# Performance work log

Hardware: AMD Instinct MI355X
Metric: run time of the kernel (lower is better)

The kernel has to match this reference:

```python
import jax, jax.numpy as jnp
from jax import lax
import numpy as np

B, T, D_IN, H, OUT = 64, 512, 512, 1024, 128


def setup_inputs() -> dict:
    key = jax.random.key(0)
    ks = jax.random.split(key, 12)
    s = 0.02
    return {
        "x": jax.random.normal(ks[0], (B, T, D_IN), dtype=jnp.float32),
        "W_ih0": jax.random.normal(ks[1], (H, D_IN), dtype=jnp.float32) * s,
        "W_hh0": jax.random.normal(ks[2], (H, H), dtype=jnp.float32) * s,
        "b_ih0": jax.random.normal(ks[3], (H,), dtype=jnp.float32) * s,
        "b_hh0": jax.random.normal(ks[4], (H,), dtype=jnp.float32) * s,
        "W_ih1": jax.random.normal(ks[5], (H, H), dtype=jnp.float32) * s,
        "W_hh1": jax.random.normal(ks[6], (H, H), dtype=jnp.float32) * s,
        "b_ih1": jax.random.normal(ks[7], (H,), dtype=jnp.float32) * s,
        "b_hh1": jax.random.normal(ks[8], (H,), dtype=jnp.float32) * s,
        "W_fc": jax.random.normal(ks[9], (OUT, H), dtype=jnp.float32) * s,
        "b_fc": jax.random.normal(ks[10], (OUT,), dtype=jnp.float32) * s,
    }


def _rnn_layer(seq, W_ih, W_hh, b_ih, b_hh):
    # seq: [B, T, D] -> outputs [B, T, H]; h_t = tanh(x_t W_ih^T + b_ih + h_{t-1} W_hh^T + b_hh)
    pre = jnp.einsum("btd,hd->bth", seq, W_ih) + b_ih + b_hh  # one big input GEMM
    h0 = jnp.zeros((seq.shape[0], W_hh.shape[0]), dtype=seq.dtype)

    def step(h, p_t):
        h_new = jnp.tanh(p_t + h @ W_hh.T)
        return h_new, h_new

    _, hs = lax.scan(step, h0, jnp.swapaxes(pre, 0, 1))  # [T, B, H]
    return jnp.swapaxes(hs, 0, 1)  # [B, T, H]


def reference(x, W_ih0, W_hh0, b_ih0, b_hh0, W_ih1, W_hh1, b_ih1, b_hh1, W_fc, b_fc):
    h1 = _rnn_layer(x, W_ih0, W_hh0, b_ih0, b_hh0)
    h2 = _rnn_layer(h1, W_ih1, W_hh1, b_ih1, b_hh1)
    last = h2[:, -1, :]  # [B, H]
    return last @ W_fc.T + b_fc  # [B, OUT]
```

## Files before the change

kernel.cpp:

```cpp
#include <hip/hip_runtime.h>
#include <stdint.h>
#include <stddef.h>

#define Bn   64
#define Tn   512
#define DINn 512
#define Hn   1024
#define OUTn 128

typedef __attribute__((ext_vector_type(4))) float f32x4;
typedef __attribute__((ext_vector_type(8))) short short8;
typedef __attribute__((ext_vector_type(4))) unsigned int u32x4;

__device__ __forceinline__ unsigned short f2bf(float f){
  unsigned int x = __builtin_bit_cast(unsigned int, f);
  x += 0x7fffu + ((x >> 16) & 1u);
  return (unsigned short)(x >> 16);
}
__device__ __forceinline__ float bf2f(unsigned short u){
  return __builtin_bit_cast(float, (unsigned int)u << 16);
}
__device__ __forceinline__ float tanh_fast(float v){
  float e = __expf(2.0f * v);
  return 1.0f - 2.0f / (e + 1.0f);
}

template<bool FAST>
__device__ __forceinline__ void st16(unsigned short* p, u32x4 v){
  if constexpr (FAST)
    asm volatile("global_store_dwordx4 %0, %1, off sc0" :: "v"(p), "v"(v) : "memory");
  else
    asm volatile("global_store_dwordx4 %0, %1, off sc0 sc1" :: "v"(p), "v"(v) : "memory");
}
__device__ __forceinline__ unsigned atom_poll(unsigned int* p){
  unsigned old, zero = 0;
  asm volatile("global_atomic_add %0, %1, %2, off sc0\n\t"
               "s_waitcnt vmcnt(0)"
               : "=&v"(old) : "v"(p), "v"(zero) : "memory");
  return old;
}
__device__ __forceinline__ void atom_poll2(unsigned int* p1, unsigned int* p2,
                                           unsigned &v1, unsigned &v2){
  unsigned zero = 0;
  asm volatile("global_atomic_add %0, %2, %4, off sc0\n\t"
               "global_atomic_add %1, %3, %4, off sc0\n\t"
               "s_waitcnt vmcnt(0)"
               : "=&v"(v1), "=&v"(v2)
               : "v"(p1), "v"(p2), "v"(zero) : "memory");
}
__device__ __forceinline__ void atom_inc(unsigned int* p){
  unsigned one = 1;
  asm volatile("global_atomic_add %0, %1, off" :: "v"(p), "v"(one) : "memory");
}
__device__ __forceinline__ unsigned ld1_sc0(const unsigned int* p){
  unsigned v;
  asm volatile("global_load_dword %0, %1, off sc0\n\t"
               "s_waitcnt vmcnt(0)" : "=&v"(v) : "v"(p) : "memory");
  return v;
}
__device__ __forceinline__ unsigned ld1_nt(const unsigned int* p){
  unsigned v;
  asm volatile("global_load_dword %0, %1, off nt\n\t"
               "s_waitcnt vmcnt(0)" : "=&v"(v) : "v"(p) : "memory");
  return v;
}
__device__ __forceinline__ void ld2_nt(const unsigned int* p1, const unsigned int* p2,
                                       unsigned &v1, unsigned &v2){
  asm volatile("global_load_dword %0, %2, off nt\n\t"
               "global_load_dword %1, %3, off nt\n\t"
               "s_waitcnt vmcnt(0)"
               : "=&v"(v1), "=&v"(v2) : "v"(p1), "v"(p2) : "memory");
}
__device__ __forceinline__ unsigned umin4(u32x4 a){
  unsigned m0 = a[0] < a[1] ? a[0] : a[1];
  unsigned m1 = a[2] < a[3] ? a[2] : a[3];
  return m0 < m1 ? m0 : m1;
}
__device__ __forceinline__ unsigned ld_line8_slow(const unsigned int* p){
  u32x4 a, b;
  asm volatile("global_load_dwordx4 %0, %2, off sc0 sc1\n\t"
               "global_load_dwordx4 %1, %3, off sc0 sc1\n\t"
               "s_waitcnt vmcnt(0)"
               : "=&v"(a), "=&v"(b) : "v"(p), "v"(p + 4) : "memory");
  unsigned ma = umin4(a), mb = umin4(b);
  return ma < mb ? ma : mb;
}
__device__ __forceinline__ void waitw_nt(const unsigned int* p, unsigned want){
  if (!want) return;
  for (int i = 0; i < (1 << 16); ++i){
    if (ld1_nt(p) >= want) return;
    if (i > 16) __builtin_amdgcn_s_sleep(1);
  }
}
__device__ __forceinline__ void waitw_nt2(const unsigned int* p1, unsigned w1,
                                          const unsigned int* p2, unsigned w2){
  if (!w1){ waitw_nt(p2, w2); return; }
  for (int i = 0; i < (1 << 16); ++i){
    unsigned v1, v2;
    ld2_nt(p1, p2, v1, v2);
    if (v1 >= w1 && v2 >= w2) return;
    if (i > 16) __builtin_amdgcn_s_sleep(1);
  }
}
template<bool FAST>
__device__ __forceinline__ void wait_one(unsigned int* fc, unsigned int* fl, unsigned wfast, unsigned wslow){
  if constexpr (FAST){
    if (!wfast) return;
    for (int i = 0; i < (1 << 16); ++i){
      if (atom_poll(fc) >= wfast) return;
      if (i > 8) __builtin_amdgcn_s_sleep(1);
    }
  } else {
    if (!wslow) return;
    for (int i = 0; i < (1 << 16); ++i){
      if (ld_line8_slow(fl) >= wslow) return;
      if (i > 16) __builtin_amdgcn_s_sleep(1);
    }
  }
}
template<bool FAST>
__device__ __forceinline__ void wait_dual(unsigned int* fc1, unsigned int* fl1, unsigned wf1, unsigned ws1,
                                          unsigned int* fc2, unsigned int* fl2, unsigned wf2, unsigned ws2){
  if constexpr (FAST){
    if (!wf2){ wait_one<true>(fc1, fl1, wf1, ws1); return; }
    for (int i = 0; i < (1 << 16); ++i){
      unsigned v1, v2;
      atom_poll2(fc1, fc2, v1, v2);
      if (v1 >= wf1 && v2 >= wf2) return;
      if (i > 8) __builtin_amdgcn_s_sleep(1);
    }
  } else {
    if (!ws2){ wait_one<false>(fc1, fl1, wf1, ws1); return; }
    for (int i = 0; i < (1 << 16); ++i){
      if (ld_line8_slow(fl1) >= ws1 && ld_line8_slow(fl2) >= ws2) return;
      if (i > 16) __builtin_amdgcn_s_sleep(1);
    }
  }
}

__device__ __forceinline__ void stage_pw(const unsigned short* src, unsigned short* dst, int lane){
  const unsigned short* p0 = src + lane*8;
  const unsigned short* p1 = p0 + 512;
  u32x4 v0, v1;
  asm volatile("global_load_dwordx4 %0, %2, off sc0\n\t"
               "global_load_dwordx4 %1, %3, off sc0\n\t"
               "s_waitcnt vmcnt(0)"
               : "=&v"(v0), "=&v"(v1) : "v"(p0), "v"(p1) : "memory");
  *(u32x4*)(dst + lane*8) = v0;
  *(u32x4*)(dst + lane*8 + 512) = v1;
}
__device__ __forceinline__ void stage_pw_pv(const unsigned short* src, unsigned short* dst, int lane,
                                            const unsigned short* p4, float* pv){
  const unsigned short* p0 = src + lane*8;
  const unsigned short* p1 = p0 + 512;
  u32x4 v0, v1; unsigned u0,u1,u2,u3;
  asm volatile(
    "global_load_dwordx4 %0, %6, off sc0\n\t"
    "global_load_dwordx4 %1, %7, off sc0\n\t"
    "global_load_ushort %2, %8, off sc0\n\t"
    "global_load_ushort %3, %9, off sc0\n\t"
    "global_load_ushort %4, %10, off sc0\n\t"
    "global_load_ushort %5, %11, off sc0\n\t"
    "s_waitcnt vmcnt(0)"
    : "=&v"(v0),"=&v"(v1),"=&v"(u0),"=&v"(u1),"=&v"(u2),"=&v"(u3)
    : "v"(p0),"v"(p1),"v"(p4),"v"(p4+8),"v"(p4+16),"v"(p4+24) : "memory");
  *(u32x4*)(dst + lane*8) = v0;
  *(u32x4*)(dst + lane*8 + 512) = v1;
  pv[0]=bf2f((unsigned short)u0); pv[1]=bf2f((unsigned short)u1);
  pv[2]=bf2f((unsigned short)u2); pv[3]=bf2f((unsigned short)u3);
}

template<bool FAST>
__device__ __forceinline__ void stage_lin(const unsigned short* base, unsigned short* hl, int tid){
  const unsigned short* p0 = base + (size_t)tid * 8;
  const unsigned short* p1 = p0 + 4096;
  u32x4 v0, v1;
  if constexpr (FAST)
    asm volatile("global_load_dwordx4 %0, %2, off sc0\n\t"
                 "global_load_dwordx4 %1, %3, off sc0\n\t"
                 "s_waitcnt vmcnt(0)"
                 : "=&v"(v0), "=&v"(v1) : "v"(p0), "v"(p1) : "memory");
  else
    asm volatile("global_load_dwordx4 %0, %2, off sc0 sc1\n\t"
                 "global_load_dwordx4 %1, %3, off sc0 sc1\n\t"
                 "s_waitcnt vmcnt(0)"
                 : "=&v"(v0), "=&v"(v1) : "v"(p0), "v"(p1) : "memory");
  *(u32x4*)((char*)hl + tid * 16) = v0;
  *(u32x4*)((char*)hl + tid * 16 + 8192) = v1;
}
template<bool FAST>
__device__ __forceinline__ void ld4_chunk(const unsigned short* p, float* pv){
  unsigned u0,u1,u2,u3;
  if constexpr (FAST)
    asm volatile("global_load_ushort %0, %4, off sc0\n\t"
                 "global_load_ushort %1, %5, off sc0\n\t"
                 "global_load_ushort %2, %6, off sc0\n\t"
                 "global_load_ushort %3, %7, off sc0\n\t"
                 "s_waitcnt vmcnt(0)"
                 : "=&v"(u0), "=&v"(u1), "=&v"(u2), "=&v"(u3)
                 : "v"(p), "v"(p + 8), "v"(p + 16), "v"(p + 24) : "memory");
  else
    asm volatile("global_load_ushort %0, %4, off sc0 sc1\n\t"
                 "global_load_ushort %1, %5, off sc0 sc1\n\t"
                 "global_load_ushort %2, %6, off sc0 sc1\n\t"
                 "global_load_ushort %3, %7, off sc0 sc1\n\t"
                 "s_waitcnt vmcnt(0)"
                 : "=&v"(u0), "=&v"(u1), "=&v"(u2), "=&v"(u3)
                 : "v"(p), "v"(p + 8), "v"(p + 16), "v"(p + 24) : "memory");
  pv[0] = bf2f((unsigned short)u0); pv[1] = bf2f((unsigned short)u1);
  pv[2] = bf2f((unsigned short)u2); pv[3] = bf2f((unsigned short)u3);
}

__device__ __forceinline__ f32x4 mfma_tile(const char* lbase, const short8* wf, int lrow, int kh){
  f32x4 a0 = {0.f,0.f,0.f,0.f}, a1 = a0, a2 = a0, a3 = a0;
  int rb = kh * 128 + lrow * 16;
#pragma unroll
  for (int kk = 0; kk < 8; ++kk)
    a0 = __builtin_amdgcn_mfma_f32_16x16x32_bf16(*(const short8*)(lbase + kk*512 + rb), wf[kk], a0, 0,0,0);
#pragma unroll
  for (int kk = 8; kk < 16; ++kk)
    a1 = __builtin_amdgcn_mfma_f32_16x16x32_bf16(*(const short8*)(lbase + kk*512 + rb), wf[kk], a1, 0,0,0);
#pragma unroll
  for (int kk = 16; kk < 24; ++kk)
    a2 = __builtin_amdgcn_mfma_f32_16x16x32_bf16(*(const short8*)(lbase + kk*512 + rb), wf[kk], a2, 0,0,0);
#pragma unroll
  for (int kk = 24; kk < 32; ++kk)
    a3 = __builtin_amdgcn_mfma_f32_16x16x32_bf16(*(const short8*)(lbase + kk*512 + rb), wf[kk], a3, 0,0,0);
  return (a0 + a1) + (a2 + a3);
}

__global__ void cvt_bf16x8(const float* __restrict__ in, unsigned short* __restrict__ out,
                           long long n8){
  long long i = (long long)blockIdx.x * blockDim.x + threadIdx.x;
  long long stride = (long long)gridDim.x * blockDim.x;
  for (; i < n8; i += stride){
    const float* p = in + i*8;
    float4 a = *(const float4*)p;
    float4 b = *(const float4*)(p+4);
    short8 v;
    v[0]=(short)f2bf(a.x); v[1]=(short)f2bf(a.y); v[2]=(short)f2bf(a.z); v[3]=(short)f2bf(a.w);
    v[4]=(short)f2bf(b.x); v[5]=(short)f2bf(b.y); v[6]=(short)f2bf(b.z); v[7]=(short)f2bf(b.w);
    *(short8*)(out + i*8) = v;
  }
}

__global__ void bias_combine(const float* __restrict__ a, const float* __restrict__ b, float* __restrict__ o,
                             const float* __restrict__ c, const float* __restrict__ d, float* __restrict__ p){
  int i = blockIdx.x * blockDim.x + threadIdx.x;
  if (i < Hn){ o[i] = a[i] + b[i]; p[i] = c[i] + d[i]; }
}

__launch_bounds__(256, 2)
__global__ void gemm_pre0(const float* __restrict__ Av, const unsigned short* __restrict__ Bm,
                          const float* __restrict__ bias, unsigned short* __restrict__ C,
                          int N, int K)
{
  __shared__ unsigned short lA[128*64];
  __shared__ unsigned short lB[128*64];
  int bn = blockIdx.x, bm = blockIdx.y;
  int m0 = bm*128, n0 = bn*128;
  int tid = threadIdx.x, lane = tid & 63, w = tid >> 6;
  int wm = (w >> 1)*64, wn = (w & 1)*64;
  int cl = lane & 15, kh = lane >> 4;

  f32x4 acc[4][4];
  f32x4 z = {0.f,0.f,0.f,0.f};
#pragma unroll
  for (int i=0;i<4;i++)
#pragma unroll
    for (int j=0;j<4;j++) acc[i][j]=z;

  for (int k0 = 0; k0 < K; k0 += 64){
    __syncthreads();
#pragma unroll
    for (int r = 0; r < 4; ++r){
      int c = r*256 + tid;
      int row = c >> 3, cof = (c & 7)*8;
      const float* ap = Av + (size_t)(m0+row)*K + k0 + cof;
      float4 a = *(const float4*)ap;
      float4 b = *(const float4*)(ap+4);
      short8 v;
      v[0]=(short)f2bf(a.x); v[1]=(short)f2bf(a.y); v[2]=(short)f2bf(a.z); v[3]=(short)f2bf(a.w);
      v[4]=(short)f2bf(b.x); v[5]=(short)f2bf(b.y); v[6]=(short)f2bf(b.z); v[7]=(short)f2bf(b.w);
      *(short8*)&lA[row*64 + cof] = v;
      const unsigned short* bp = Bm + (size_t)(n0+row)*K + k0 + cof;
      *(short8*)&lB[row*64 + cof] = *(const short8*)bp;
    }
    __syncthreads();
#pragma unroll
    for (int kk = 0; kk < 2; ++kk){
      int kb = kk*32 + kh*8;
      short8 af[4], bfr[4];
#pragma unroll
      for (int i=0;i<4;i++) af[i]  = *(const short8*)&lA[(wm + i*16 + cl)*64 + kb];
#pragma unroll
      for (int j=0;j<4;j++) bfr[j] = *(const short8*)&lB[(wn + j*16 + cl)*64 + kb];
#pragma unroll
      for (int i=0;i<4;i++)
#pragma unroll
        for (int j=0;j<4;j++)
          acc[i][j] = __builtin_amdgcn_mfma_f32_16x16x32_bf16(af[i], bfr[j], acc[i][j], 0,0,0);
    }
  }
#pragma unroll
  for (int j=0;j<4;j++){
    int n = n0 + wn + j*16 + cl;
    float bs = bias[n];
#pragma unroll
    for (int i=0;i<4;i++){
      int mr = m0 + wm + i*16 + kh*4;
#pragma unroll
      for (int e=0;e<4;e++){
        int m = mr + e;
        int b = m >> 9, t = m & (Tn-1);
        C[((size_t)t*Bn + b)*N + n] = f2bf(acc[i][j][e] + bs);
      }
    }
  }
}

template<int MODE>
__device__ __forceinline__ void rnn_body(
    int role, int g, int slot, int tid, int w, int lane, int cl, int kh, int lrow,
    const unsigned short* pre0, unsigned short* bufP, unsigned short* h1buf,
    const float* bias1,
    unsigned int* FCA0, unsigned int* FCA1, unsigned int* FCB, unsigned int* FCC,
    unsigned int* FLA, unsigned int* FLB, unsigned int* FLC,
    unsigned int* FNA, unsigned int* FNB, unsigned int* FNC,
    const short8* wf, unsigned short* hl, unsigned short* outl)
{
  constexpr bool FAST = (MODE < 2);
  const char* lbase = (const char*)hl;
  int n0 = slot*128 + w*16;
  int olocal = w*128 + ((cl>>3)*8 + kh*4)*8 + (cl&7);
  int khc = kh & 1;
  unsigned int* myFL = ((role == 0) ? FLA : (role == 1) ? FLB : FLC) + slot;
  unsigned int* myFN = ((role == 0) ? FNA : (role == 1) ? FNB : FNC) + slot;

  for (int t = 0; t < Tn; ++t){
    float pv[4] = {0.f,0.f,0.f,0.f};
    if (role == 0 && kh < 2){
      const unsigned short* pp = pre0 + ((size_t)t*Bn + g*8 + kh*4)*Hn + n0 + cl;
#pragma unroll
      for (int j=0;j<4;j++) pv[j] = bf2f(pp[(size_t)j*Hn]);
    }
    bool staged = true;
    if constexpr (MODE == 0){
      if (role == 0){
        if (t > 0){
          waitw_nt(FNA + w, (unsigned)t);
          stage_pw(h1buf + ((size_t)(t+1)*8 + g)*8192 + w*1024, hl + w*1024, lane);
        } else staged = false;
      } else if (role == 1){
        waitw_nt(FNA + w, (unsigned)(t+1));
        stage_pw(h1buf + ((size_t)(t+2)*8 + g)*8192 + w*1024, hl + w*1024, lane);
      } else {
        const unsigned short* pA = h1buf + ((size_t)t*8 + g)*8192 + slot*1024
                                   + ((w*16+cl)>>3)*64 + khc*32 + (cl&7);
        if (t > 0){
          waitw_nt2(FNC + w, (unsigned)t, FNB + slot, (unsigned)(t+1));
          stage_pw_pv(bufP + ((size_t)(t-1)*Bn + g*8)*Hn + w*1024, hl + w*1024, lane, pA, pv);
        } else {
          staged = false;
          waitw_nt(FNB + slot, 1u);
          ld4_chunk<true>(pA, pv);
        }
      }
    } else {
      if (tid == 0){
        if (role == 0)      wait_one <FAST>(FCA0, FLA, 8u*(unsigned)t, (unsigned)t);
        else if (role == 1) wait_one <FAST>(FCA1, FLA, 8u*(unsigned)(t+1), (unsigned)(t+1));
        else                wait_dual<FAST>(FCB, FLB, 8u*(unsigned)(t+1), (unsigned)(t+1),
                                            FCC, FLC, 8u*(unsigned)t, (unsigned)t);
      }
      __syncthreads();
      if (role == 0){
        if (t > 0) stage_lin<FAST>(h1buf + ((size_t)(t+1)*8 + g)*8192, hl, tid);
        else staged = false;
      } else if (role == 1){
        stage_lin<FAST>(h1buf + ((size_t)(t+2)*8 + g)*8192, hl, tid);
      } else {
        if (kh < 2)
          ld4_chunk<FAST>(h1buf + ((size_t)t*8 + g)*8192 + slot*1024 + ((w*16+cl)>>3)*64 + kh*32 + (cl&7), pv);
        if (t > 0) stage_lin<FAST>(bufP + ((size_t)(t-1)*Bn + g*8)*Hn, hl, tid);
        else staged = false;
      }
    }
    __syncthreads();
    f32x4 acc = {0.f,0.f,0.f,0.f};
    if (staged) acc = mfma_tile(lbase, wf, lrow, kh);
    if (kh < 2){
      float bs = (role == 1) ? bias1[n0 + cl] : 0.f;
#pragma unroll
      for (int j=0;j<4;j++){
        float v = acc[j] + pv[j] + bs;
        if (role != 1) v = tanh_fast(v);
        outl[olocal + j*8] = f2bf(v);
      }
    }
    unsigned short* tile;
    if (role == 0)      tile = h1buf + ((size_t)(t+2)*8 + g)*8192;
    else if (role == 1) tile = h1buf + ((size_t)t*8 + g)*8192;
    else                tile = bufP + ((size_t)t*Bn + g*8)*Hn;
    if (lane < 16){
      u32x4 v = *(const u32x4*)(outl + w*128 + lane*8);
      st16<FAST>(tile + slot*1024 + (w*16 + lane)*8, v);
    }
    asm volatile("s_waitcnt vmcnt(0)" ::: "memory");
    __syncthreads();
    if (tid == 0){
      if constexpr (MODE == 0){
        asm volatile("global_store_dword %0, %1, off sc0" :: "v"(myFN), "v"((unsigned)(t+1)) : "memory");
      } else if constexpr (MODE == 1){
        if (role == 0){ atom_inc(FCA0); atom_inc(FCA1); }
        else if (role == 1) atom_inc(FCB);
        else atom_inc(FCC);
      } else {
        asm volatile("global_store_dword %0, %1, off sc0 sc1" :: "v"(myFL), "v"((unsigned)(t+1)) : "memory");
      }
    }
  }
}

__launch_bounds__(512, 2)
__global__ void rnn_fused(const unsigned short* __restrict__ pre0_ro,
                          unsigned short* __restrict__ bufP,
                          unsigned short* __restrict__ h1buf,
                          const float* __restrict__ Whh0,
                          const float* __restrict__ Wih1,
                          const float* __restrict__ Whh1,
                          const float* __restrict__ bias1,
                          unsigned int* ctrs)
{
  __shared__ __align__(16) unsigned short hl[8192];
  __shared__ __align__(16) unsigned short outl[1024];
  __shared__ int s_mode;
  int bx = blockIdx.x;
  int g = bx & 7;
  int sub = bx >> 3;
  int role = sub >> 3, slot = sub & 7;
  int tid = threadIdx.x, lane = tid & 63, w = tid >> 6;
  int n0 = slot*128 + w*16;
  int cl = lane & 15, kh = lane >> 4, lrow = cl & 7;
  unsigned int* FLA = ctrs + (0*8 + g)*32;
  unsigned int* FLB = ctrs + (1*8 + g)*32;
  unsigned int* FLC = ctrs + (2*8 + g)*32;
  unsigned int* arrive1 = ctrs + 768;
  unsigned int* badAT   = ctrs + 772;
  unsigned int* arrive2 = ctrs + 776;
  unsigned int* badNT   = ctrs + 780;
  unsigned int* arrive3 = ctrs + 784;
  unsigned int* FCA0 = ctrs + 1536 + (0*8 + g)*32;
  unsigned int* FCB  = ctrs + 1536 + (1*8 + g)*32;
  unsigned int* FCC  = ctrs + 1536 + (2*8 + g)*32;
  unsigned int* FCA1 = ctrs + 1536 + (3*8 + g)*32;
  unsigned int* FNA = ctrs + 2560 + (0*8 + g)*32;
  unsigned int* FNB = ctrs + 2560 + (1*8 + g)*32;
  unsigned int* FNC = ctrs + 2560 + (2*8 + g)*32;

  if (tid == 0){
    int xcc;
    asm volatile("s_getreg_b32 %0, hwreg(HW_REG_XCC_ID)" : "=s"(xcc));
    unsigned int* atw = ctrs + 1024 + g*32;  unsigned int* atarmed = atw + 16;
    unsigned int* ntw = ctrs + 3328 + g*32;  unsigned int* ntarmed = ntw + 16;
    if (xcc != g){
      __hip_atomic_fetch_or(badNT, 1u, __ATOMIC_RELAXED, __HIP_MEMORY_SCOPE_AGENT);
      __hip_atomic_fetch_or(badAT, 1u, __ATOMIC_RELAXED, __HIP_MEMORY_SCOPE_AGENT);
    }
    unsigned pr = ld1_nt(ntw) + ld1_nt(ntarmed);
    asm volatile("" :: "v"(pr));
    __hip_atomic_fetch_add(arrive1, 1u, __ATOMIC_ACQ_REL, __HIP_MEMORY_SCOPE_AGENT);
    int t1 = 0;
    for (int i = 0; i < (1 << 20); ++i){
      if (__hip_atomic_load(arrive1, __ATOMIC_ACQUIRE, __HIP_MEMORY_SCOPE_AGENT) >= 192u){ t1 = 1; break; }
      __builtin_amdgcn_s_sleep(2);
    }
    if (!t1){
      __hip_atomic_fetch_or(badNT, 1u, __ATOMIC_RELAXED, __HIP_MEMORY_SCOPE_AGENT);
      __hip_atomic_fetch_or(badAT, 1u, __ATOMIC_RELAXED, __HIP_MEMORY_SCOPE_AGENT);
    }
    unsigned magicN = 0xBEEF0000u | (unsigned)g;
    if (sub == 0){
      asm volatile("global_store_dword %0, %1, off sc0\n\t"
                   "s_waitcnt vmcnt(0)\n\t"
                   "global_store_dword %2, %3, off sc0"
                   :: "v"(ntw), "v"(magicN), "v"(ntarmed), "v"(1u) : "memory");
    }
    int okN = 0;
    for (int i = 0; i < (1 << 14); ++i){
      if (ld1_nt(ntarmed) == 1u){ okN = (ld1_nt(ntw) == magicN); break; }
      if (i > 8) __builtin_amdgcn_s_sleep(1);
    }
    if (!okN) __hip_atomic_fetch_or(badNT, 1u, __ATOMIC_RELAXED, __HIP_MEMORY_SCOPE_AGENT);
    __hip_atomic_fetch_add(arrive2, 1u, __ATOMIC_ACQ_REL, __HIP_MEMORY_SCOPE_AGENT);
    int t2 = 0;
    for (int i = 0; i < (1 << 20); ++i){
      if (__hip_atomic_load(arrive2, __ATOMIC_ACQUIRE, __HIP_MEMORY_SCOPE_AGENT) >= 192u){ t2 = 1; break; }
      __builtin_amdgcn_s_sleep(2);
    }
    if (!t2){
      __hip_atomic_fetch_or(badNT, 1u, __ATOMIC_RELAXED, __HIP_MEMORY_SCOPE_AGENT);
      __hip_atomic_fetch_or(badAT, 1u, __ATOMIC_RELAXED, __HIP_MEMORY_SCOPE_AGENT);
    }
    unsigned magicA = 0xCAFE0000u | (unsigned)g;
    if (sub == 0){
      asm volatile("global_store_dword %0, %1, off sc0\n\t"
                   "s_waitcnt vmcnt(0)" :: "v"(atw), "v"(magicA) : "memory");
      atom_inc(atarmed);
    }
    int okA = 0;
    for (int i = 0; i < (1 << 15); ++i){
      if (atom_poll(atarmed) >= 1u){ okA = (ld1_sc0(atw) == magicA); break; }
      if (i > 16) __builtin_amdgcn_s_sleep(1);
    }
    if (!okA) __hip_atomic_fetch_or(badAT, 1u, __ATOMIC_RELAXED, __HIP_MEMORY_SCOPE_AGENT);
    __hip_atomic_fetch_add(arrive3, 1u, __ATOMIC_ACQ_REL, __HIP_MEMORY_SCOPE_AGENT);
    int t3 = 0;
    for (int i = 0; i < (1 << 20); ++i){
      if (__hip_atomic_load(arrive3, __ATOMIC_ACQUIRE, __HIP_MEMORY_SCOPE_AGENT) >= 192u){ t3 = 1; break; }
      __builtin_amdgcn_s_sleep(2);
    }
    unsigned bN = __hip_atomic_load(badNT, __ATOMIC_ACQUIRE, __HIP_MEMORY_SCOPE_AGENT);
    unsigned bA = __hip_atomic_load(badAT, __ATOMIC_ACQUIRE, __HIP_MEMORY_SCOPE_AGENT);
    s_mode = (!t3) ? 2 : (bN == 0u ? 0 : (bA == 0u ? 1 : 2));
  }
  __syncthreads();
  const int mode = s_mode;

  const float* Wmat = (role == 0) ? Whh0 : (role == 1) ? Wih1 : Whh1;
  short8 wf[32];
  {
    const float* wr = Wmat + (size_t)(n0 + cl)*Hn + kh*8;
#pragma unroll
    for (int kk = 0; kk < 32; ++kk){
      float4 a = *(const float4*)(wr + kk*32);
      float4 b = *(const float4*)(wr + kk*32 + 4);
      short8 v;
      v[0]=(short)f2bf(a.x); v[1]=(short)f2bf(a.y); v[2]=(short)f2bf(a.z); v[3]=(short)f2bf(a.w);
      v[4]=(short)f2bf(b.x); v[5]=(short)f2bf(b.y); v[6]=(short)f2bf(b.z); v[7]=(short)f2bf(b.w);
      wf[kk] = v;
    }
  }

  if (mode == 0)
    rnn_body<0>(role, g, slot, tid, w, lane, cl, kh, lrow, pre0_ro, bufP, h1buf,
                bias1, FCA0, FCA1, FCB, FCC, FLA, FLB, FLC, FNA, FNB, FNC, wf, hl, outl);
  else if (mode == 1)
    rnn_body<1>(role, g, slot, tid, w, lane, cl, kh, lrow, pre0_ro, bufP, h1buf,
                bias1, FCA0, FCA1, FCB, FCC, FLA, FLB, FLC, FNA, FNB, FNC, wf, hl, outl);
  else
    rnn_body<2>(role, g, slot, tid, w, lane, cl, kh, lrow, pre0_ro, bufP, h1buf,
                bias1, FCA0, FCA1, FCB, FCC, FLA, FLB, FLC, FNA, FNB, FNC, wf, hl, outl);
}

__global__ void fc_k(const unsigned short* __restrict__ bufP,
                     const float* __restrict__ Wfc, const float* __restrict__ bfc,
                     float* __restrict__ out)
{
  int gw = (blockIdx.x * blockDim.x + threadIdx.x) >> 6;
  int lane = threadIdx.x & 63;
  int b = gw >> 7, o = gw & 127;
  const unsigned short* tile = bufP + ((size_t)(Tn-1)*Bn + (b & ~7))*Hn;
  int r = b & 7;
  const float* wr = Wfc + (size_t)o*Hn;
  float s = 0.f;
  for (int k = lane; k < Hn; k += 64)
    s += bf2f(tile[((k>>3)*8 + r)*8 + (k&7)]) * wr[k];
#pragma unroll
  for (int off = 32; off > 0; off >>= 1) s += __shfl_down(s, off, 64);
  if (lane == 0) out[b*OUTn + o] = s + bfc[o];
}

extern "C" void kernel_launch(void* const* d_in, const int* in_sizes, int n_in,
                              void* d_out, int out_size, void* d_ws, size_t ws_size,
                              hipStream_t stream)
{
  const float* x    = (const float*)d_in[0];
  const float* Wih0 = (const float*)d_in[1];
  const float* Whh0 = (const float*)d_in[2];
  const float* bih0 = (const float*)d_in[3];
  const float* bhh0 = (const float*)d_in[4];
  const float* Wih1 = (const float*)d_in[5];
  const float* Whh1 = (const float*)d_in[6];
  const float* bih1 = (const float*)d_in[7];
  const float* bhh1 = (const float*)d_in[8];
  const float* Wfc  = (const float*)d_in[9];
  const float* bfc  = (const float*)d_in[10];
  float* out = (float*)d_out;

  unsigned short* bufP  = (unsigned short*)d_ws;
  unsigned short* h1buf = bufP  + (size_t)Bn*Tn*Hn;
  unsigned short* wih0b = h1buf + (size_t)(Tn+2)*8*8192;
  float* bias0 = (float*)(wih0b + (size_t)Hn*DINn);
  float* bias1 = bias0 + Hn;
  unsigned int* ctrs = (unsigned int*)(bias1 + Hn);

  hipMemsetAsync(ctrs, 0, 4096*sizeof(unsigned int), stream);

  cvt_bf16x8<<<256, 256, 0, stream>>>(Wih0, wih0b, (long long)Hn*DINn/8);
  bias_combine<<<4, 256, 0, stream>>>(bih0, bhh0, bias0, bih1, bhh1, bias1);

  dim3 g1(Hn/128, (Bn*Tn)/128);
  gemm_pre0<<<g1, 256, 0, stream>>>(x, wih0b, bias0, bufP, Hn, DINn);

  rnn_fused<<<192, 512, 0, stream>>>(bufP, bufP, h1buf, Whh0, Wih1, Whh1, bias1, ctrs);

  fc_k<<<2048, 256, 0, stream>>>(bufP, Wfc, bfc, out);
}
```

Baseline: 1.148 ms.

## Replace flag-based inter-block sync with poisoned-buffer data polling in RNN pipeline

Adds a mode where the h1, pre1 and h2 buffers are pre-filled with 0xFFFF (a NaN bf16 pattern), and consumers poll the data itself with non-temporal loads until no poison values remain. This removes per-step flag stores and flag waits, and drops the vmcnt wait before the barrier. Intermediate layer-1 and h2 tensors move into separate write-once buffers, which needs extra workspace and three extra memsets per call. Correctness rests on 0xFFFF never occurring as a real value and on 16-byte stores being observed atomically.

```diff
diff --git a/kernel.cpp b/kernel.cpp
--- a/kernel.cpp
+++ b/kernel.cpp
@@ -24,6 +24,8 @@
   float e = __expf(2.0f * v);
   return 1.0f - 2.0f / (e + 1.0f);
 }
+
+#define LGKM_BAR() asm volatile("s_waitcnt lgkmcnt(0)\ns_barrier" ::: "memory")
 
 template<bool FAST>
 __device__ __forceinline__ void st16(unsigned short* p, u32x4 v){
@@ -136,6 +138,48 @@
       if (i > 16) __builtin_amdgcn_s_sleep(1);
     }
   }
+}
+
+__device__ __forceinline__ bool chk8(u32x4 v){
+  bool ok = true;
+#pragma unroll
+  for (int d = 0; d < 4; ++d){
+    ok = ok && ((v[d] & 0xFFFFu) != 0xFFFFu) && ((v[d] >> 16) != 0xFFFFu);
+  }
+  return ok;
+}
+__device__ __forceinline__ void poison_stage(const unsigned short* src, unsigned short* dst, int lane){
+  const unsigned short* p0 = src + lane*8;
+  const unsigned short* p1 = p0 + 512;
+  u32x4 v0, v1;
+  bool ok = false;
+  for (int i = 0; i < (1 << 16) && !ok; ++i){
+    asm volatile("global_load_dwordx4 %0, %2, off nt\n\t"
+                 "global_load_dwordx4 %1, %3, off nt\n\t"
+                 "s_waitcnt vmcnt(0)"
+                 : "=&v"(v0), "=&v"(v1) : "v"(p0), "v"(p1) : "memory");
+    ok = chk8(v0) && chk8(v1);
+    if (!ok && i > 4) __builtin_amdgcn_s_sleep(1);
+  }
+  *(u32x4*)(dst + lane*8) = v0;
+  *(u32x4*)(dst + lane*8 + 512) = v1;
+}
+__device__ __forceinline__ void poison_pv(const unsigned short* p, float* pv, bool active){
+  unsigned u0 = 0, u1 = 0, u2 = 0, u3 = 0;
+  bool ok = !active;
+  for (int i = 0; i < (1 << 16) && !ok; ++i){
+    asm volatile("global_load_ushort %0, %4, off nt\n\t"
+                 "global_load_ushort %1, %5, off nt\n\t"
+                 "global_load_ushort %2, %6, off nt\n\t"
+                 "global_load_ushort %3, %7, off nt\n\t"
+                 "s_waitcnt vmcnt(0)"
+                 : "=&v"(u0), "=&v"(u1), "=&v"(u2), "=&v"(u3)
+                 : "v"(p), "v"(p + 8), "v"(p + 16), "v"(p + 24) : "memory");
+    ok = (u0 != 0xFFFFu) && (u1 != 0xFFFFu) && (u2 != 0xFFFFu) && (u3 != 0xFFFFu);
+    if (!ok && i > 4) __builtin_amdgcn_s_sleep(1);
+  }
+  pv[0] = bf2f((unsigned short)u0); pv[1] = bf2f((unsigned short)u1);
+  pv[2] = bf2f((unsigned short)u2); pv[3] = bf2f((unsigned short)u3);
 }
 
 __device__ __forceinline__ void stage_pw(const unsigned short* src, unsigned short* dst, int lane){
@@ -319,11 +363,11 @@
   }
 }
 
-template<int MODE>
+template<int MODE, bool POISON>
 __device__ __forceinline__ void rnn_body(
     int role, int g, int slot, int tid, int w, int lane, int cl, int kh, int lrow,
-    const unsigned short* pre0, unsigned short* bufP, unsigned short* h1buf,
-    const float* bias1,
+    const unsigned short* pre0, unsigned short* h1base, unsigned short* pre1base,
+    unsigned short* h2base, const float* bias1,
     unsigned int* FCA0, unsigned int* FCA1, unsigned int* FCB, unsigned int* FCC,
     unsigned int* FLA, unsigned int* FLB, unsigned int* FLC,
     unsigned int* FNA, unsigned int* FNB, unsigned int* FNC,
@@ -345,21 +389,34 @@
       for (int j=0;j<4;j++) pv[j] = bf2f(pp[(size_t)j*Hn]);
     }
     bool staged = true;
-    if constexpr (MODE == 0){
+    if constexpr (MODE == 0 && POISON){
+      if (role == 0){
+        if (t > 0) poison_stage(h1base + ((size_t)(t+1)*8 + g)*8192 + w*1024, hl + w*1024, lane);
+        else staged = false;
+      } else if (role == 1){
+        poison_stage(h1base + ((size_t)(t+2)*8 + g)*8192 + w*1024, hl + w*1024, lane);
+      } else {
+        const unsigned short* pA = pre1base + ((size_t)t*8 + g)*8192 + slot*1024
+                                   + ((w*16+cl)>>3)*64 + khc*32 + (cl&7);
+        if (t > 0) poison_stage(h2base + ((size_t)(t-1)*8 + g)*8192 + w*1024, hl + w*1024, lane);
+        else staged = false;
+        poison_pv(pA, pv, kh < 2);
+      }
+    } else if constexpr (MODE == 0){
       if (role == 0){
         if (t > 0){
           waitw_nt(FNA + w, (unsigned)t);
-          stage_pw(h1buf + ((size_t)(t+1)*8 + g)*8192 + w*1024, hl + w*1024, lane);
+          stage_pw(h1base + ((size_t)(t+1)*8 + g)*8192 + w*1024, hl + w*1024, lane);
         } else staged = false;
       } else if (role == 1){
         waitw_nt(FNA + w, (unsigned)(t+1));
-        stage_pw(h1buf + ((size_t)(t+2)*8 + g)*8192 + w*1024, hl + w*1024, lane);
+        stage_pw(h1base + ((size_t)(t+2)*8 + g)*8192 + w*1024, hl + w*1024, lane);
       } else {
-        const unsigned short* pA = h1buf + ((size_t)t*8 + g)*8192 + slot*1024
+        const unsigned short* pA = pre1base + ((size_t)t*8 + g)*8192 + slot*1024
                                    + ((w*16+cl)>>3)*64 + khc*32 + (cl&7);
         if (t > 0){
           waitw_nt2(FNC + w, (unsigned)t, FNB + slot, (unsigned)(t+1));
-          stage_pw_pv(bufP + ((size_t)(t-1)*Bn + g*8)*Hn + w*1024, hl + w*1024, lane, pA, pv);
+          stage_pw_pv(h2base + ((size_t)(t-1)*8 + g)*8192 + w*1024, hl + w*1024, lane, pA, pv);
         } else {
           staged = false;
           waitw_nt(FNB + slot, 1u);
@@ -375,18 +432,19 @@
       }
       __syncthreads();
       if (role == 0){
-        if (t > 0) stage_lin<FAST>(h1buf + ((size_t)(t+1)*8 + g)*8192, hl, tid);
+        if (t > 0) stage_lin<FAST>(h1base + ((size_t)(t+1)*8 + g)*8192, hl, tid);
         else staged = false;
       } else if (role == 1){
-        stage_lin<FAST>(h1buf + ((size_t)(t+2)*8 + g)*8192, hl, tid);
+        stage_lin<FAST>(h1base + ((size_t)(t+2)*8 + g)*8192, hl, tid);
       } else {
         if (kh < 2)
-          ld4_chunk<FAST>(h1buf + ((size_t)t*8 + g)*8192 + slot*1024 + ((w*16+cl)>>3)*64 + kh*32 + (cl&7), pv);
-        if (t > 0) stage_lin<FAST>(bufP + ((size_t)(t-1)*Bn + g*8)*Hn, hl, tid);
+          ld4_chunk<FAST>(pre1base + ((size_t)t*8 + g)*8192 + slot*1024 + ((w*16+cl)>>3)*64 + kh*32 + (cl&7), pv);
+        if (t > 0) stage_lin<FAST>(h2base + ((size_t)(t-1)*8 + g)*8192, hl, tid);
         else staged = false;
       }
     }
-    __syncthreads();
+    if constexpr (MODE == 0 && POISON) LGKM_BAR();
+    else __syncthreads();
     f32x4 acc = {0.f,0.f,0.f,0.f};
     if (staged) acc = mfma_tile(lbase, wf, lrow, kh);
     if (kh < 2){
@@ -399,24 +457,30 @@
       }
     }
     unsigned short* tile;
-    if (role == 0)      tile = h1buf + ((size_t)(t+2)*8 + g)*8192;
-    else if (role == 1) tile = h1buf + ((size_t)t*8 + g)*8192;
-    else                tile = bufP + ((size_t)t*Bn + g*8)*Hn;
+    if (role == 0)      tile = h1base + ((size_t)(t+2)*8 + g)*8192;
+    else if (role == 1) tile = pre1base + ((size_t)t*8 + g)*8192;
+    else                tile = h2base + ((size_t)t*8 + g)*8192;
     if (lane < 16){
       u32x4 v = *(const u32x4*)(outl + w*128 + lane*8);
       st16<FAST>(tile + slot*1024 + (w*16 + lane)*8, v);
     }
-    asm volatile("s_waitcnt vmcnt(0)" ::: "memory");
-    __syncthreads();
-    if (tid == 0){
+    if constexpr (MODE == 0 && POISON){
+      LGKM_BAR();
+    } else {
+      asm volatile("s_waitcnt vmcnt(0)" ::: "memory");
+      __syncthreads();
       if constexpr (MODE == 0){
-        asm volatile("global_store_dword %0, %1, off sc0" :: "v"(myFN), "v"((unsigned)(t+1)) : "memory");
+        if (lane == 0 && w == 0)
+          asm volatile("global_store_dword %0, %1, off sc0" :: "v"(myFN), "v"((unsigned)(t+1)) : "memory");
       } else if constexpr (MODE == 1){
-        if (role == 0){ atom_inc(FCA0); atom_inc(FCA1); }
-        else if (role == 1) atom_inc(FCB);
-        else atom_inc(FCC);
+        if (tid == 0){
+          if (role == 0){ atom_inc(FCA0); atom_inc(FCA1); }
+          else if (role == 1) atom_inc(FCB);
+          else atom_inc(FCC);
+        }
       } else {
-        asm volatile("global_store_dword %0, %1, off sc0 sc1" :: "v"(myFL), "v"((unsigned)(t+1)) : "memory");
+        if (tid == 0)
+          asm volatile("global_store_dword %0, %1, off sc0 sc1" :: "v"(myFL), "v"((unsigned)(t+1)) : "memory");
       }
     }
   }
@@ -424,13 +488,14 @@
 
 __launch_bounds__(512, 2)
 __global__ void rnn_fused(const unsigned short* __restrict__ pre0_ro,
-                          unsigned short* __restrict__ bufP,
-                          unsigned short* __restrict__ h1buf,
+                          unsigned short* __restrict__ h1base,
+                          unsigned short* __restrict__ pre1base,
+                          unsigned short* __restrict__ h2base,
                           const float* __restrict__ Whh0,
                           const float* __restrict__ Wih1,
                           const float* __restrict__ Whh1,
                           const float* __restrict__ bias1,
-                          unsigned int* ctrs)
+                          unsigned int* ctrs, int allowPoison)
 {
   __shared__ __align__(16) unsigned short hl[8192];
   __shared__ __align__(16) unsigned short outl[1024];
@@ -542,25 +607,28 @@
     }
   }
 
-  if (mode == 0)
-    rnn_body<0>(role, g, slot, tid, w, lane, cl, kh, lrow, pre0_ro, bufP, h1buf,
-                bias1, FCA0, FCA1, FCB, FCC, FLA, FLB, FLC, FNA, FNB, FNC, wf, hl, outl);
+  if (mode == 0 && allowPoison)
+    rnn_body<0,true >(role, g, slot, tid, w, lane, cl, kh, lrow, pre0_ro, h1base, pre1base, h2base,
+                      bias1, FCA0, FCA1, FCB, FCC, FLA, FLB, FLC, FNA, FNB, FNC, wf, hl, outl);
+  else if (mode == 0)
+    rnn_body<0,false>(role, g, slot, tid, w, lane, cl, kh, lrow, pre0_ro, h1base, pre1base, h2base,
+                      bias1, FCA0, FCA1, FCB, FCC, FLA, FLB, FLC, FNA, FNB, FNC, wf, hl, outl);
   else if (mode == 1)
-    rnn_body<1>(role, g, slot, tid, w, lane, cl, kh, lrow, pre0_ro, bufP, h1buf,
-                bias1, FCA0, FCA1, FCB, FCC, FLA, FLB, FLC, FNA, FNB, FNC, wf, hl, outl);
+    rnn_body<1,false>(role, g, slot, tid, w, lane, cl, kh, lrow, pre0_ro, h1base, pre1base, h2base,
+                      bias1, FCA0, FCA1, FCB, FCC, FLA, FLB, FLC, FNA, FNB, FNC, wf, hl, outl);
   else
-    rnn_body<2>(role, g, slot, tid, w, lane, cl, kh, lrow, pre0_ro, bufP, h1buf,
-                bias1, FCA0, FCA1, FCB, FCC, FLA, FLB, FLC, FNA, FNB, FNC, wf, hl, outl);
-}
-
-__global__ void fc_k(const unsigned short* __restrict__ bufP,
+    rnn_body<2,false>(role, g, slot, tid, w, lane, cl, kh, lrow, pre0_ro, h1base, pre1base, h2base,
+                      bias1, FCA0, FCA1, FCB, FCC, FLA, FLB, FLC, FNA, FNB, FNC, wf, hl, outl);
+}
+
+__global__ void fc_k(const unsigned short* __restrict__ h2base,
                      const float* __restrict__ Wfc, const float* __restrict__ bfc,
                      float* __restrict__ out)
 {
   int gw = (blockIdx.x * blockDim.x + threadIdx.x) >> 6;
   int lane = threadIdx.x & 63;
   int b = gw >> 7, o = gw & 127;
-  const unsigned short* tile = bufP + ((size_t)(Tn-1)*Bn + (b & ~7))*Hn;
+  const unsigned short* tile = h2base + ((size_t)(Tn-1)*8 + (b>>3))*8192;
   int r = b & 7;
   const float* wr = Wfc + (size_t)o*Hn;
   float s = 0.f;
@@ -588,22 +656,47 @@
   const float* bfc  = (const float*)d_in[10];
   float* out = (float*)d_out;
 
+  const size_t nP  = (size_t)Bn*Tn*Hn;
+  const size_t nH1 = (size_t)(Tn+2)*8*8192;
+  const size_t nT  = (size_t)Tn*8*8192;
+  const size_t nW  = (size_t)Hn*DINn;
+
+  size_t needP = (nP + nH1 + 2*nT + nW)*2 + 2*Hn*sizeof(float) + 8192*sizeof(unsigned);
+  int poison = (ws_size >= needP + 4096) ? 1 : 0;
+
   unsigned short* bufP  = (unsigned short*)d_ws;
-  unsigned short* h1buf = bufP  + (size_t)Bn*Tn*Hn;
-  unsigned short* wih0b = h1buf + (size_t)(Tn+2)*8*8192;
-  float* bias0 = (float*)(wih0b + (size_t)Hn*DINn);
+  unsigned short* h1buf = bufP  + nP;
+  unsigned short* pre1b;
+  unsigned short* h2b;
+  unsigned short* wih0b;
+  if (poison){
+    pre1b = h1buf + nH1;
+    h2b   = pre1b + nT;
+    wih0b = h2b + nT;
+  } else {
+    pre1b = h1buf;
+    h2b   = bufP;
+    wih0b = h1buf + nH1;
+  }
+  float* bias0 = (float*)(wih0b + nW);
   float* bias1 = bias0 + Hn;
   unsigned int* ctrs = (unsigned int*)(bias1 + Hn);
 
   hipMemsetAsync(ctrs, 0, 4096*sizeof(unsigned int), stream);
-
-  cvt_bf16x8<<<256, 256, 0, stream>>>(Wih0, wih0b, (long long)Hn*DINn/8);
+  if (poison){
+    hipMemsetAsync(h1buf, 0xFF, nH1*2, stream);
+    hipMemsetAsync(pre1b, 0xFF, nT*2, stream);
+    hipMemsetAsync(h2b,   0xFF, nT*2, stream);
+  }
+
+  cvt_bf16x8<<<256, 256, 0, stream>>>(Wih0, wih0b, (long long)(nW/8));
   bias_combine<<<4, 256, 0, stream>>>(bih0, bhh0, bias0, bih1, bhh1, bias1);
 
   dim3 g1(Hn/128, (Bn*Tn)/128);
   gemm_pre0<<<g1, 256, 0, stream>>>(x, wih0b, bias0, bufP, Hn, DINn);
 
-  rnn_fused<<<192, 512, 0, stream>>>(bufP, bufP, h1buf, Whh0, Wih1, Whh1, bias1, ctrs);
-
-  fc_k<<<2048, 256, 0, stream>>>(bufP, Wfc, bfc, out);
-}
+  rnn_fused<<<192, 512, 0, stream>>>(bufP, h1buf, pre1b, h2b,
+                                     Whh0, Wih1, Whh1, bias1, ctrs, poison);
+
+  fc_k<<<2048, 256, 0, stream>>>(h2b, Wfc, bfc, out);
+}
```

Measured after the change: 1.148 ms. About the same (-0.0%).

## Use per-wave ready flags and double-buffered LDS in MODE 0 RNN pipeline

Applied to the files above, without the earlier changes.

In the MODE 0 path, each wave now publishes its own progress flag, and consumers poll a line of 8 per-wave flags with vector loads and take their minimum. This replaces the block-wide __syncthreads plus single-thread flag store at the end of each step. The shared staging buffer hl is doubled and alternated by step parity, so a fast wave can stage the next step without overwriting data slower waves are still reading. This removes a block barrier per timestep at the cost of more LDS, wider poll loads, and a relocated counter layout that must not overlap other control words.

```diff
diff --git a/kernel.cpp b/kernel.cpp
--- a/kernel.cpp
+++ b/kernel.cpp
@@ -64,17 +64,19 @@
                "s_waitcnt vmcnt(0)" : "=&v"(v) : "v"(p) : "memory");
   return v;
 }
-__device__ __forceinline__ void ld2_nt(const unsigned int* p1, const unsigned int* p2,
-                                       unsigned &v1, unsigned &v2){
-  asm volatile("global_load_dword %0, %2, off nt\n\t"
-               "global_load_dword %1, %3, off nt\n\t"
-               "s_waitcnt vmcnt(0)"
-               : "=&v"(v1), "=&v"(v2) : "v"(p1), "v"(p2) : "memory");
-}
 __device__ __forceinline__ unsigned umin4(u32x4 a){
   unsigned m0 = a[0] < a[1] ? a[0] : a[1];
   unsigned m1 = a[2] < a[3] ? a[2] : a[3];
   return m0 < m1 ? m0 : m1;
+}
+__device__ __forceinline__ unsigned ld_line8_nt(const unsigned int* p){
+  u32x4 a, b;
+  asm volatile("global_load_dwordx4 %0, %2, off nt\n\t"
+               "global_load_dwordx4 %1, %3, off nt\n\t"
+               "s_waitcnt vmcnt(0)"
+               : "=&v"(a), "=&v"(b) : "v"(p), "v"(p + 4) : "memory");
+  unsigned ma = umin4(a), mb = umin4(b);
+  return ma < mb ? ma : mb;
 }
 __device__ __forceinline__ unsigned ld_line8_slow(const unsigned int* p){
   u32x4 a, b;
@@ -85,20 +87,28 @@
   unsigned ma = umin4(a), mb = umin4(b);
   return ma < mb ? ma : mb;
 }
-__device__ __forceinline__ void waitw_nt(const unsigned int* p, unsigned want){
+__device__ __forceinline__ void wait8_nt(const unsigned int* p, unsigned want){
   if (!want) return;
   for (int i = 0; i < (1 << 16); ++i){
-    if (ld1_nt(p) >= want) return;
+    if (ld_line8_nt(p) >= want) return;
     if (i > 16) __builtin_amdgcn_s_sleep(1);
   }
 }
-__device__ __forceinline__ void waitw_nt2(const unsigned int* p1, unsigned w1,
+__device__ __forceinline__ void wait8_nt2(const unsigned int* p1, unsigned w1,
                                           const unsigned int* p2, unsigned w2){
-  if (!w1){ waitw_nt(p2, w2); return; }
+  if (!w1){ wait8_nt(p2, w2); return; }
   for (int i = 0; i < (1 << 16); ++i){
-    unsigned v1, v2;
-    ld2_nt(p1, p2, v1, v2);
-    if (v1 >= w1 && v2 >= w2) return;
+    u32x4 a, b, c, d;
+    asm volatile("global_load_dwordx4 %0, %4, off nt\n\t"
+                 "global_load_dwordx4 %1, %5, off nt\n\t"
+                 "global_load_dwordx4 %2, %6, off nt\n\t"
+                 "global_load_dwordx4 %3, %7, off nt\n\t"
+                 "s_waitcnt vmcnt(0)"
+                 : "=&v"(a), "=&v"(b), "=&v"(c), "=&v"(d)
+                 : "v"(p1), "v"(p1 + 4), "v"(p2), "v"(p2 + 4) : "memory");
+    unsigned m1 = umin4(a) < umin4(b) ? umin4(a) : umin4(b);
+    unsigned m2 = umin4(c) < umin4(d) ? umin4(c) : umin4(d);
+    if (m1 >= w1 && m2 >= w2) return;
     if (i > 16) __builtin_amdgcn_s_sleep(1);
   }
 }
@@ -330,14 +340,16 @@
     const short8* wf, unsigned short* hl, unsigned short* outl)
 {
   constexpr bool FAST = (MODE < 2);
-  const char* lbase = (const char*)hl;
   int n0 = slot*128 + w*16;
   int olocal = w*128 + ((cl>>3)*8 + kh*4)*8 + (cl&7);
   int khc = kh & 1;
   unsigned int* myFL = ((role == 0) ? FLA : (role == 1) ? FLB : FLC) + slot;
-  unsigned int* myFN = ((role == 0) ? FNA : (role == 1) ? FNB : FNC) + slot;
+  unsigned int* myFN = ((role == 0) ? FNA : (role == 1) ? FNB : FNC) + slot*8 + w;
 
   for (int t = 0; t < Tn; ++t){
+    unsigned short* hlb = (MODE == 0) ? hl + (t & 1)*8192 : hl;
+    const char* lbase = (const char*)hlb;
+
     float pv[4] = {0.f,0.f,0.f,0.f};
     if (role == 0 && kh < 2){
       const unsigned short* pp = pre0 + ((size_t)t*Bn + g*8 + kh*4)*Hn + n0 + cl;
@@ -348,21 +360,21 @@
     if constexpr (MODE == 0){
       if (role == 0){
         if (t > 0){
-          waitw_nt(FNA + w, (unsigned)t);
-          stage_pw(h1buf + ((size_t)(t+1)*8 + g)*8192 + w*1024, hl + w*1024, lane);
+          wait8_nt(FNA + w*8, (unsigned)t);
+          stage_pw(h1buf + ((size_t)(t+1)*8 + g)*8192 + w*1024, hlb + w*1024, lane);
         } else staged = false;
       } else if (role == 1){
-        waitw_nt(FNA + w, (unsigned)(t+1));
-        stage_pw(h1buf + ((size_t)(t+2)*8 + g)*8192 + w*1024, hl + w*1024, lane);
+        wait8_nt(FNA + w*8, (unsigned)(t+1));
+        stage_pw(h1buf + ((size_t)(t+2)*8 + g)*8192 + w*1024, hlb + w*1024, lane);
       } else {
         const unsigned short* pA = h1buf + ((size_t)t*8 + g)*8192 + slot*1024
                                    + ((w*16+cl)>>3)*64 + khc*32 + (cl&7);
         if (t > 0){
-          waitw_nt2(FNC + w, (unsigned)t, FNB + slot, (unsigned)(t+1));
-          stage_pw_pv(bufP + ((size_t)(t-1)*Bn + g*8)*Hn + w*1024, hl + w*1024, lane, pA, pv);
+          wait8_nt2(FNC + w*8, (unsigned)t, FNB + slot*8, (unsigned)(t+1));
+          stage_pw_pv(bufP + ((size_t)(t-1)*Bn + g*8)*Hn + w*1024, hlb + w*1024, lane, pA, pv);
         } else {
           staged = false;
-          waitw_nt(FNB + slot, 1u);
+          wait8_nt(FNB + slot*8, 1u);
           ld4_chunk<true>(pA, pv);
         }
       }
@@ -375,14 +387,14 @@
       }
       __syncthreads();
       if (role == 0){
-        if (t > 0) stage_lin<FAST>(h1buf + ((size_t)(t+1)*8 + g)*8192, hl, tid);
+        if (t > 0) stage_lin<FAST>(h1buf + ((size_t)(t+1)*8 + g)*8192, hlb, tid);
         else staged = false;
       } else if (role == 1){
-        stage_lin<FAST>(h1buf + ((size_t)(t+2)*8 + g)*8192, hl, tid);
+        stage_lin<FAST>(h1buf + ((size_t)(t+2)*8 + g)*8192, hlb, tid);
       } else {
         if (kh < 2)
           ld4_chunk<FAST>(h1buf + ((size_t)t*8 + g)*8192 + slot*1024 + ((w*16+cl)>>3)*64 + kh*32 + (cl&7), pv);
-        if (t > 0) stage_lin<FAST>(bufP + ((size_t)(t-1)*Bn + g*8)*Hn, hl, tid);
+        if (t > 0) stage_lin<FAST>(bufP + ((size_t)(t-1)*Bn + g*8)*Hn, hlb, tid);
         else staged = false;
       }
     }
@@ -406,17 +418,21 @@
       u32x4 v = *(const u32x4*)(outl + w*128 + lane*8);
       st16<FAST>(tile + slot*1024 + (w*16 + lane)*8, v);
     }
-    asm volatile("s_waitcnt vmcnt(0)" ::: "memory");
-    __syncthreads();
-    if (tid == 0){
-      if constexpr (MODE == 0){
+    if constexpr (MODE == 0){
+      asm volatile("s_waitcnt vmcnt(0)" ::: "memory");
+      if (lane == 0)
         asm volatile("global_store_dword %0, %1, off sc0" :: "v"(myFN), "v"((unsigned)(t+1)) : "memory");
-      } else if constexpr (MODE == 1){
-        if (role == 0){ atom_inc(FCA0); atom_inc(FCA1); }
-        else if (role == 1) atom_inc(FCB);
-        else atom_inc(FCC);
-      } else {
-        asm volatile("global_store_dword %0, %1, off sc0 sc1" :: "v"(myFL), "v"((unsigned)(t+1)) : "memory");
+    } else {
+      asm volatile("s_waitcnt vmcnt(0)" ::: "memory");
+      __syncthreads();
+      if (tid == 0){
+        if constexpr (MODE == 1){
+          if (role == 0){ atom_inc(FCA0); atom_inc(FCA1); }
+          else if (role == 1) atom_inc(FCB);
+          else atom_inc(FCC);
+        } else {
+          asm volatile("global_store_dword %0, %1, off sc0 sc1" :: "v"(myFL), "v"((unsigned)(t+1)) : "memory");
+        }
       }
     }
   }
@@ -432,7 +448,7 @@
                           const float* __restrict__ bias1,
                           unsigned int* ctrs)
 {
-  __shared__ __align__(16) unsigned short hl[8192];
+  __shared__ __align__(16) unsigned short hl[16384];
   __shared__ __align__(16) unsigned short outl[1024];
   __shared__ int s_mode;
   int bx = blockIdx.x;
@@ -454,15 +470,15 @@
   unsigned int* FCB  = ctrs + 1536 + (1*8 + g)*32;
   unsigned int* FCC  = ctrs + 1536 + (2*8 + g)*32;
   unsigned int* FCA1 = ctrs + 1536 + (3*8 + g)*32;
-  unsigned int* FNA = ctrs + 2560 + (0*8 + g)*32;
-  unsigned int* FNB = ctrs + 2560 + (1*8 + g)*32;
-  unsigned int* FNC = ctrs + 2560 + (2*8 + g)*32;
+  unsigned int* FNA = ctrs + 2560 + (0*8 + g)*64;
+  unsigned int* FNB = ctrs + 2560 + (1*8 + g)*64;
+  unsigned int* FNC = ctrs + 2560 + (2*8 + g)*64;
 
   if (tid == 0){
     int xcc;
     asm volatile("s_getreg_b32 %0, hwreg(HW_REG_XCC_ID)" : "=s"(xcc));
     unsigned int* atw = ctrs + 1024 + g*32;  unsigned int* atarmed = atw + 16;
-    unsigned int* ntw = ctrs + 3328 + g*32;  unsigned int* ntarmed = ntw + 16;
+    unsigned int* ntw = ctrs + 1280 + g*32;  unsigned int* ntarmed = ntw + 16;
     if (xcc != g){
       __hip_atomic_fetch_or(badNT, 1u, __ATOMIC_RELAXED, __HIP_MEMORY_SCOPE_AGENT);
       __hip_atomic_fetch_or(badAT, 1u, __ATOMIC_RELAXED, __HIP_MEMORY_SCOPE_AGENT);
```

After: 1.127 ms, median of 2. Within noise of the previous version (-1.9%).
